# Optimization experiments

Measured on AMD Instinct MI355X. Metric: run time of the kernel, lower is better.

## Reference

```python
import jax, jax.numpy as jnp
import numpy as np

D, N_EXP, TOP_K = 2048, 64, 8
B, S = 4, 4096

def setup_inputs() -> dict:
    key = jax.random.key(0)
    k1, k2, k3, k4 = jax.random.split(key, 4)
    hidden_states = jax.random.normal(k1, (B, S, D), dtype=jnp.float32)
    # nn.Linear weights are [out, in]; default init ~ U(-1/sqrt(d), 1/sqrt(d))
    bound = 1.0 / np.sqrt(D)
    W_gate = jax.random.uniform(k2, (N_EXP, D), jnp.float32, -bound, bound)
    W_noise = 0.01 * jax.random.normal(k3, (N_EXP, D), dtype=jnp.float32)
    # training-mode noise (router_step % top_k == 0 path): fixed-seed randn
    noise = jax.random.normal(k4, (B, S, N_EXP), dtype=jnp.float32)
    return {"hidden_states": hidden_states, "W_gate": W_gate,
            "W_noise": W_noise, "noise": noise}

def reference(hidden_states, W_gate, W_noise, noise):
    # logits = h @ W_gate^T  : [B,S,n_exp]
    logits = jnp.einsum('bsd,ed->bse', hidden_states, W_gate)
    scale = jax.nn.softplus(jnp.einsum('bsd,ed->bse', hidden_states, W_noise))
    logits = logits + noise * scale
    gates = jax.nn.softmax(logits, axis=-1)
    vals, inds = jax.lax.top_k(gates, TOP_K)  # sorted desc (torch used sorted=False)
    return vals, inds, gates
```

## Files before the change

### kernel.cpp

```cpp
#include <hip/hip_runtime.h>
#include <math.h>

typedef __attribute__((ext_vector_type(8))) _Float16 half8;
typedef __attribute__((ext_vector_type(4))) float    f32x4;

constexpr int D_DIM = 2048;
constexpr int NEXP  = 64;
constexpr int TOPK  = 8;
constexpr int NTOK  = 16384;
constexpr int TM    = 32;
constexpr int BK    = 128;
constexpr int NCH   = D_DIM / BK;
constexpr int OSTR  = 132;
constexpr float WSCALE  = 4096.0f;
constexpr float INV_WSC = 1.0f / 4096.0f;

__device__ __forceinline__ unsigned short f16b(float x) {
    _Float16 h = (_Float16)x;
    return __builtin_bit_cast(unsigned short, h);
}
__device__ __forceinline__ float f16tof(unsigned short b) {
    return (float)__builtin_bit_cast(_Float16, b);
}

__global__ void prep_w(const float* __restrict__ Wg, const float* __restrict__ Wn,
                       unsigned short* __restrict__ wsB)
{
    const int idx = blockIdx.x * blockDim.x + threadIdx.x;
    const int n   = idx >> 8;
    const int K8  = idx & 255;
    const float* src = (n < 64) ? (Wg + (size_t)n * D_DIM)
                                : (Wn + (size_t)(n - 64) * D_DIM);
    float4 a = *reinterpret_cast<const float4*>(src + K8 * 8);
    float4 b = *reinterpret_cast<const float4*>(src + K8 * 8 + 4);

    float v[8] = {a.x, a.y, a.z, a.w, b.x, b.y, b.z, b.w};
    union { unsigned short u[8]; half8 s; } H, L;
#pragma unroll
    for (int j = 0; j < 8; ++j) {
        float xs = v[j] * WSCALE;
        unsigned short h = f16b(xs);
        H.u[j] = h;
        L.u[j] = f16b(xs - f16tof(h));
    }
    const int l = ((K8 & 3) * 16) + (n & 15);
    const size_t base = (size_t)(K8 >> 2) * 8192 + (size_t)(n >> 4) * 1024 + (size_t)l * 8;
    *reinterpret_cast<half8*>(wsB + base)       = H.s;
    *reinterpret_cast<half8*>(wsB + base + 512) = L.s;
}

__global__ __launch_bounds__(512, 4)
void noisy_topk_router(const float* __restrict__ hs,
                       const unsigned short* __restrict__ wsB,
                       const float* __restrict__ nz,
                       float* __restrict__ out)
{
    __shared__ __align__(16) char smem[32768];
    unsigned short* stage  = reinterpret_cast<unsigned short*>(smem);
    float*          logits = reinterpret_cast<float*>(smem);

    const int tid  = threadIdx.x;
    const int lane = tid & 63;
    const int w    = tid >> 6;
    const int t0   = blockIdx.x * TM;

    const int j0r = lane >> 4;
    const int mr  = lane & 15;

    const int r    = tid >> 4;
    const int q    = tid & 15;
    const int ks_s = q >> 2;
    const int j0s  = q & 3;
    const int ms   = r & 15;
    const int mts  = r >> 4;
    const int fs   = ks_s | ((j0s & 1) << 2);
    const int wroff = (mts * 4 + ks_s) * 512 + (j0s * 16 + (ms ^ fs)) * 8;
    const float* hrow = hs + (size_t)(t0 + r) * D_DIM + q * 8;

    const unsigned short* bbase = wsB + (size_t)w * 1024 + (size_t)lane * 8;

    f32x4 accP0[2], accP1[2], accX0[2], accX1[2];
#pragma unroll
    for (int mt = 0; mt < 2; ++mt) {
        accP0[mt] = (f32x4){0.f, 0.f, 0.f, 0.f};
        accP1[mt] = (f32x4){0.f, 0.f, 0.f, 0.f};
        accX0[mt] = (f32x4){0.f, 0.f, 0.f, 0.f};
        accX1[mt] = (f32x4){0.f, 0.f, 0.f, 0.f};
    }

    auto cvt_write = [&](float4 a, float4 b, unsigned short* buf) {
        float v[8] = {a.x, a.y, a.z, a.w, b.x, b.y, b.z, b.w};
        union { unsigned short u[8]; half8 s; } H, L;
#pragma unroll
        for (int j = 0; j < 8; ++j) {
            unsigned short h = f16b(v[j]);
            H.u[j] = h;
            L.u[j] = f16b(v[j] - f16tof(h));
        }
        *reinterpret_cast<half8*>(buf + wroff)        = H.s;
        *reinterpret_cast<half8*>(buf + wroff + 4096) = L.s;
    };

    {
        float4 a = *reinterpret_cast<const float4*>(hrow);
        float4 b = *reinterpret_cast<const float4*>(hrow + 4);
        cvt_write(a, b, stage);
    }
    __syncthreads();

#pragma unroll 1
    for (int c = 0; c < NCH; ++c) {
        half8 bh[4], bl[4];
#pragma unroll
        for (int ks = 0; ks < 4; ++ks) {
            const unsigned short* bp = bbase + (size_t)(c * 4 + ks) * 8192;
            bh[ks] = *reinterpret_cast<const half8*>(bp);
            bl[ks] = *reinterpret_cast<const half8*>(bp + 512);
        }
        __builtin_amdgcn_sched_barrier(0);

        float4 pa, pb;
        if (c + 1 < NCH) {
            pa = *reinterpret_cast<const float4*>(hrow + (c + 1) * BK);
            pb = *reinterpret_cast<const float4*>(hrow + (c + 1) * BK + 4);
        }
        __builtin_amdgcn_sched_barrier(0);

        const unsigned short* sb = stage + (c & 1) * 8192;
#pragma unroll
        for (int ks = 0; ks < 4; ++ks) {
            const int fr = ks | ((j0r & 1) << 2);
#pragma unroll
            for (int mt = 0; mt < 2; ++mt) {
                const int off = (mt * 4 + ks) * 512 + (j0r * 16 + (mr ^ fr)) * 8;
                half8 ahi = *reinterpret_cast<const half8*>(sb + off);
                half8 alo = *reinterpret_cast<const half8*>(sb + off + 4096);
                if ((ks & 1) == 0)
                    accP0[mt] = __builtin_amdgcn_mfma_f32_16x16x32_f16(ahi, bh[ks], accP0[mt], 0, 0, 0);
                else
                    accP1[mt] = __builtin_amdgcn_mfma_f32_16x16x32_f16(ahi, bh[ks], accP1[mt], 0, 0, 0);
                accX0[mt] = __builtin_amdgcn_mfma_f32_16x16x32_f16(ahi, bl[ks], accX0[mt], 0, 0, 0);
                accX1[mt] = __builtin_amdgcn_mfma_f32_16x16x32_f16(alo, bh[ks], accX1[mt], 0, 0, 0);
            }
        }

        if (c + 1 < NCH)
            cvt_write(pa, pb, stage + ((c + 1) & 1) * 8192);
        __syncthreads();
    }

    {
        const int colb = w * 16 + mr;
#pragma unroll
        for (int mt = 0; mt < 2; ++mt) {
            const int rowb = mt * 16 + j0r * 4;
#pragma unroll
            for (int rr = 0; rr < 4; ++rr)
                logits[(rowb + rr) * OSTR + colb] =
                    (accP0[mt][rr] + accP1[mt][rr] + accX0[mt][rr] + accX1[mt][rr]) * INV_WSC;
        }
    }
    __syncthreads();

    float* gout = out + (size_t)NTOK * TOPK * 2;
    for (int tt = 0; tt < 4; ++tt) {
        const int tl  = w * 4 + tt;
        const int tok = t0 + tl;
        float gsc = logits[tl * OSTR + lane];
        float nl  = logits[tl * OSTR + 64 + lane];
        float nzv = nz[(size_t)tok * NEXP + lane];
        float sp  = fmaxf(nl, 0.0f) + log1pf(expf(-fabsf(nl)));
        float le  = fmaf(nzv, sp, gsc);

        float mx = le;
#pragma unroll
        for (int d = 32; d > 0; d >>= 1) mx = fmaxf(mx, __shfl_xor(mx, d));
        float pe = expf(le - mx);
        float s  = pe;
#pragma unroll
        for (int d = 32; d > 0; d >>= 1) s += __shfl_xor(s, d);
        float g = pe * (1.0f / s);

        gout[(size_t)tok * NEXP + lane] = g;

        float v = g;
        float keepv = 0.0f;
        int   keepi = 0;
#pragma unroll
        for (int it = 0; it < TOPK; ++it) {
            float m  = v;
            int   mi = lane;
#pragma unroll
            for (int d = 32; d > 0; d >>= 1) {
                float om = __shfl_xor(m, d);
                int   oi = __shfl_xor(mi, d);
                bool take = (om > m) || (om == m && oi < mi);
                m  = take ? om : m;
                mi = take ? oi : mi;
            }
            if (lane == it) { keepv = m; keepi = mi; }
            if (lane == mi) v = -1.0f;
        }
        if (lane < TOPK) {
            out[(size_t)tok * TOPK + lane] = keepv;
            out[(size_t)NTOK * TOPK + (size_t)tok * TOPK + lane] = (float)keepi;
        }
    }
}

extern "C" void kernel_launch(void* const* d_in, const int* in_sizes, int n_in,
                              void* d_out, int out_size, void* d_ws, size_t ws_size,
                              hipStream_t stream) {
    const float* hs = (const float*)d_in[0];
    const float* Wg = (const float*)d_in[1];
    const float* Wn = (const float*)d_in[2];
    const float* nz = (const float*)d_in[3];
    float* out = (float*)d_out;
    unsigned short* wsB = (unsigned short*)d_ws;

    prep_w<<<64, 512, 0, stream>>>(Wg, Wn, wsB);
    noisy_topk_router<<<NTOK / TM, 512, 0, stream>>>(hs, wsB, nz, out);
}
```

Baseline: 229.9 us.

## Switch router GEMM to 32x32x16 MFMA with 64-token tiles and double-buffered B

Reworks the logits GEMM to use 32x32x16 f16 MFMA instructions with a 64-token block tile and 64-wide K chunks. The weight layout is rebuilt to match, and the main loop is unrolled by two to double-buffer the weight fragments in registers. Hidden-state and noise loads become nontemporal. The larger tiles should cut weight reloads per token and MFMA issue overhead, at the cost of lower occupancy (launch bounds go from 4 to 2) and higher register pressure.

```diff
diff --git a/kernel.cpp b/kernel.cpp
--- a/kernel.cpp
+++ b/kernel.cpp
@@ -1,15 +1,16 @@
 #include <hip/hip_runtime.h>
 #include <math.h>
 
-typedef __attribute__((ext_vector_type(8))) _Float16 half8;
-typedef __attribute__((ext_vector_type(4))) float    f32x4;
+typedef __attribute__((ext_vector_type(8)))  _Float16 half8;
+typedef __attribute__((ext_vector_type(4)))  float    f32x4;
+typedef __attribute__((ext_vector_type(16))) float    f32x16;
 
 constexpr int D_DIM = 2048;
 constexpr int NEXP  = 64;
 constexpr int TOPK  = 8;
 constexpr int NTOK  = 16384;
-constexpr int TM    = 32;
-constexpr int BK    = 128;
+constexpr int TM    = 64;
+constexpr int BK    = 64;
 constexpr int NCH   = D_DIM / BK;
 constexpr int OSTR  = 132;
 constexpr float WSCALE  = 4096.0f;
@@ -21,6 +22,9 @@
 }
 __device__ __forceinline__ float f16tof(unsigned short b) {
     return (float)__builtin_bit_cast(_Float16, b);
+}
+__device__ __forceinline__ f32x4 ntload4(const float* p) {
+    return __builtin_nontemporal_load(reinterpret_cast<const f32x4*>(p));
 }
 
 __global__ void prep_w(const float* __restrict__ Wg, const float* __restrict__ Wn,
@@ -31,10 +35,10 @@
     const int K8  = idx & 255;
     const float* src = (n < 64) ? (Wg + (size_t)n * D_DIM)
                                 : (Wn + (size_t)(n - 64) * D_DIM);
-    float4 a = *reinterpret_cast<const float4*>(src + K8 * 8);
-    float4 b = *reinterpret_cast<const float4*>(src + K8 * 8 + 4);
-
-    float v[8] = {a.x, a.y, a.z, a.w, b.x, b.y, b.z, b.w};
+    f32x4 a = *reinterpret_cast<const f32x4*>(src + K8 * 8);
+    f32x4 b = *reinterpret_cast<const f32x4*>(src + K8 * 8 + 4);
+
+    float v[8] = {a[0], a[1], a[2], a[3], b[0], b[1], b[2], b[3]};
     union { unsigned short u[8]; half8 s; } H, L;
 #pragma unroll
     for (int j = 0; j < 8; ++j) {
@@ -43,53 +47,60 @@
         H.u[j] = h;
         L.u[j] = f16b(xs - f16tof(h));
     }
-    const int l = ((K8 & 3) * 16) + (n & 15);
-    const size_t base = (size_t)(K8 >> 2) * 8192 + (size_t)(n >> 4) * 1024 + (size_t)l * 8;
+    const int kk   = K8 >> 1;
+    const int koct = K8 & 1;
+    const int lane = koct * 32 + (n & 31);
+    const size_t base = (size_t)kk * 4096 + (size_t)(n >> 5) * 1024 + (size_t)lane * 8;
     *reinterpret_cast<half8*>(wsB + base)       = H.s;
     *reinterpret_cast<half8*>(wsB + base + 512) = L.s;
 }
 
-__global__ __launch_bounds__(512, 4)
+__global__ __launch_bounds__(512, 2)
 void noisy_topk_router(const float* __restrict__ hs,
                        const unsigned short* __restrict__ wsB,
                        const float* __restrict__ nz,
                        float* __restrict__ out)
 {
-    __shared__ __align__(16) char smem[32768];
+    __shared__ __align__(16) char smem[33792];
     unsigned short* stage  = reinterpret_cast<unsigned short*>(smem);
     float*          logits = reinterpret_cast<float*>(smem);
 
     const int tid  = threadIdx.x;
     const int lane = tid & 63;
     const int w    = tid >> 6;
+    const int mt   = w & 1;
+    const int nt   = w >> 1;
     const int t0   = blockIdx.x * TM;
 
-    const int j0r = lane >> 4;
-    const int mr  = lane & 15;
-
-    const int r    = tid >> 4;
-    const int q    = tid & 15;
-    const int ks_s = q >> 2;
-    const int j0s  = q & 3;
-    const int ms   = r & 15;
-    const int mts  = r >> 4;
-    const int fs   = ks_s | ((j0s & 1) << 2);
-    const int wroff = (mts * 4 + ks_s) * 512 + (j0s * 16 + (ms ^ fs)) * 8;
+    const int lxr = lane ^ ((lane >> 5) << 2);
+
+    const int r    = tid >> 3;
+    const int q    = tid & 7;
+    const int ks_w = q >> 1;
+    const int koct = q & 1;
+    const int uphys = ((koct << 5) + (r & 31)) ^ ks_w ^ (koct << 2);
+    const int woff  = (ks_w * 2 + (r >> 5)) * 1024 + uphys * 8;
     const float* hrow = hs + (size_t)(t0 + r) * D_DIM + q * 8;
 
-    const unsigned short* bbase = wsB + (size_t)w * 1024 + (size_t)lane * 8;
-
-    f32x4 accP0[2], accP1[2], accX0[2], accX1[2];
-#pragma unroll
-    for (int mt = 0; mt < 2; ++mt) {
-        accP0[mt] = (f32x4){0.f, 0.f, 0.f, 0.f};
-        accP1[mt] = (f32x4){0.f, 0.f, 0.f, 0.f};
-        accX0[mt] = (f32x4){0.f, 0.f, 0.f, 0.f};
-        accX1[mt] = (f32x4){0.f, 0.f, 0.f, 0.f};
-    }
-
-    auto cvt_write = [&](float4 a, float4 b, unsigned short* buf) {
-        float v[8] = {a.x, a.y, a.z, a.w, b.x, b.y, b.z, b.w};
+    const unsigned short* bbase = wsB + (size_t)nt * 1024 + (size_t)lane * 8;
+
+    f32x16 accP, accX0, accX1;
+#pragma unroll
+    for (int i = 0; i < 16; ++i) { accP[i] = 0.f; accX0[i] = 0.f; accX1[i] = 0.f; }
+
+    half8 bh0[4], bl0[4], bh1[4], bl1[4];
+
+    auto loadB = [&](int chunk, half8* bh, half8* bl) {
+#pragma unroll
+        for (int ks = 0; ks < 4; ++ks) {
+            const unsigned short* p = bbase + (size_t)(chunk * 4 + ks) * 4096;
+            bh[ks] = *reinterpret_cast<const half8*>(p);
+            bl[ks] = *reinterpret_cast<const half8*>(p + 512);
+        }
+    };
+
+    auto cvt_write = [&](f32x4 a, f32x4 b, unsigned short* buf) {
+        float v[8] = {a[0], a[1], a[2], a[3], b[0], b[1], b[2], b[3]};
         union { unsigned short u[8]; half8 s; } H, L;
 #pragma unroll
         for (int j = 0; j < 8; ++j) {
@@ -97,78 +108,71 @@
             H.u[j] = h;
             L.u[j] = f16b(v[j] - f16tof(h));
         }
-        *reinterpret_cast<half8*>(buf + wroff)        = H.s;
-        *reinterpret_cast<half8*>(buf + wroff + 4096) = L.s;
+        *reinterpret_cast<half8*>(buf + woff)       = H.s;
+        *reinterpret_cast<half8*>(buf + woff + 512) = L.s;
     };
 
+    auto body = [&](const half8* bh, const half8* bl, const unsigned short* sb) {
+#pragma unroll
+        for (int ks = 0; ks < 4; ++ks) {
+            const int off = (ks * 2 + mt) * 1024 + (lxr ^ ks) * 8;
+            half8 ahi = *reinterpret_cast<const half8*>(sb + off);
+            half8 alo = *reinterpret_cast<const half8*>(sb + off + 512);
+            accP  = __builtin_amdgcn_mfma_f32_32x32x16_f16(ahi, bh[ks], accP,  0, 0, 0);
+            accX0 = __builtin_amdgcn_mfma_f32_32x32x16_f16(ahi, bl[ks], accX0, 0, 0, 0);
+            accX1 = __builtin_amdgcn_mfma_f32_32x32x16_f16(alo, bh[ks], accX1, 0, 0, 0);
+        }
+    };
+
+    loadB(0, bh0, bl0);
+    cvt_write(ntload4(hrow), ntload4(hrow + 4), stage);
+    __syncthreads();
+
+#pragma unroll 1
+    for (int cc = 0; cc < NCH / 2; ++cc) {
+        const int e = 2 * cc;
+        loadB(e + 1, bh1, bl1);
+        __builtin_amdgcn_sched_barrier(0);
+        f32x4 pa = ntload4(hrow + (e + 1) * BK);
+        f32x4 pb = ntload4(hrow + (e + 1) * BK + 4);
+        __builtin_amdgcn_sched_barrier(0);
+        body(bh0, bl0, stage);
+        cvt_write(pa, pb, stage + 8192);
+        __syncthreads();
+
+        const bool more = (e + 2) < NCH;
+        f32x4 pa2, pb2;
+        if (more) {
+            loadB(e + 2, bh0, bl0);
+            __builtin_amdgcn_sched_barrier(0);
+            pa2 = ntload4(hrow + (e + 2) * BK);
+            pb2 = ntload4(hrow + (e + 2) * BK + 4);
+            __builtin_amdgcn_sched_barrier(0);
+        }
+        body(bh1, bl1, stage + 8192);
+        if (more)
+            cvt_write(pa2, pb2, stage);
+        __syncthreads();
+    }
+
     {
-        float4 a = *reinterpret_cast<const float4*>(hrow);
-        float4 b = *reinterpret_cast<const float4*>(hrow + 4);
-        cvt_write(a, b, stage);
+        const int colb  = nt * 32 + (lane & 31);
+        const int rbase = mt * 32 + 4 * (lane >> 5);
+#pragma unroll
+        for (int rr = 0; rr < 16; ++rr) {
+            const int row = rbase + (rr & 3) + 8 * (rr >> 2);
+            logits[row * OSTR + colb] = (accP[rr] + accX0[rr] + accX1[rr]) * INV_WSC;
+        }
     }
     __syncthreads();
 
-#pragma unroll 1
-    for (int c = 0; c < NCH; ++c) {
-        half8 bh[4], bl[4];
-#pragma unroll
-        for (int ks = 0; ks < 4; ++ks) {
-            const unsigned short* bp = bbase + (size_t)(c * 4 + ks) * 8192;
-            bh[ks] = *reinterpret_cast<const half8*>(bp);
-            bl[ks] = *reinterpret_cast<const half8*>(bp + 512);
-        }
-        __builtin_amdgcn_sched_barrier(0);
-
-        float4 pa, pb;
-        if (c + 1 < NCH) {
-            pa = *reinterpret_cast<const float4*>(hrow + (c + 1) * BK);
-            pb = *reinterpret_cast<const float4*>(hrow + (c + 1) * BK + 4);
-        }
-        __builtin_amdgcn_sched_barrier(0);
-
-        const unsigned short* sb = stage + (c & 1) * 8192;
-#pragma unroll
-        for (int ks = 0; ks < 4; ++ks) {
-            const int fr = ks | ((j0r & 1) << 2);
-#pragma unroll
-            for (int mt = 0; mt < 2; ++mt) {
-                const int off = (mt * 4 + ks) * 512 + (j0r * 16 + (mr ^ fr)) * 8;
-                half8 ahi = *reinterpret_cast<const half8*>(sb + off);
-                half8 alo = *reinterpret_cast<const half8*>(sb + off + 4096);
-                if ((ks & 1) == 0)
-                    accP0[mt] = __builtin_amdgcn_mfma_f32_16x16x32_f16(ahi, bh[ks], accP0[mt], 0, 0, 0);
-                else
-                    accP1[mt] = __builtin_amdgcn_mfma_f32_16x16x32_f16(ahi, bh[ks], accP1[mt], 0, 0, 0);
-                accX0[mt] = __builtin_amdgcn_mfma_f32_16x16x32_f16(ahi, bl[ks], accX0[mt], 0, 0, 0);
-                accX1[mt] = __builtin_amdgcn_mfma_f32_16x16x32_f16(alo, bh[ks], accX1[mt], 0, 0, 0);
-            }
-        }
-
-        if (c + 1 < NCH)
-            cvt_write(pa, pb, stage + ((c + 1) & 1) * 8192);
-        __syncthreads();
-    }
-
-    {
-        const int colb = w * 16 + mr;
-#pragma unroll
-        for (int mt = 0; mt < 2; ++mt) {
-            const int rowb = mt * 16 + j0r * 4;
-#pragma unroll
-            for (int rr = 0; rr < 4; ++rr)
-                logits[(rowb + rr) * OSTR + colb] =
-                    (accP0[mt][rr] + accP1[mt][rr] + accX0[mt][rr] + accX1[mt][rr]) * INV_WSC;
-        }
-    }
-    __syncthreads();
-
     float* gout = out + (size_t)NTOK * TOPK * 2;
-    for (int tt = 0; tt < 4; ++tt) {
-        const int tl  = w * 4 + tt;
+    for (int tt = 0; tt < 8; ++tt) {
+        const int tl  = w * 8 + tt;
         const int tok = t0 + tl;
         float gsc = logits[tl * OSTR + lane];
         float nl  = logits[tl * OSTR + 64 + lane];
-        float nzv = nz[(size_t)tok * NEXP + lane];
+        float nzv = __builtin_nontemporal_load(nz + (size_t)tok * NEXP + lane);
         float sp  = fmaxf(nl, 0.0f) + log1pf(expf(-fabsf(nl)));
         float le  = fmaf(nzv, sp, gsc);
 
```

After: 254.5 us. 1.11x slower.
